# Kernel tuning notes

Measured on AMD Instinct MI355X. Metric: run time of the kernel, lower is better.

Reference implementation:

```python
import jax, jax.numpy as jnp
import numpy as np

BITS = 3
LEVELS = 2 ** BITS            # 8
HALF_RANGE = (LEVELS - 1) / 2  # 3.5
INCREMENT = 1.0 / (LEVELS // 2)  # 0.25


def setup_inputs() -> dict:
    key = jax.random.key(0)
    kq, kk, kv, kr = jax.random.split(key, 4)
    B, H, S, D = 2, 16, 2048, 128
    q = jax.random.normal(kq, (B, H, S, D), dtype=jnp.float32)
    k = jax.random.normal(kk, (B, H, S, D), dtype=jnp.float32)
    v = jax.random.normal(kv, (B, H, S, D), dtype=jnp.float32)
    # random orthogonal rotation (QR of a Gaussian), as in PolarQuant.__init__
    Hmat = jax.random.normal(kr, (D, D), dtype=jnp.float32)
    R, _ = jnp.linalg.qr(Hmat)
    qjl_scale = jnp.full((1,), 0.01, dtype=jnp.float32)
    return {"q": q, "k": k, "v": v, "R": R, "qjl_scale": qjl_scale}


def _compress_decompress(x, R, qjl_scale):
    """PolarQuant rotate -> QJL 3-bit quantize (+ sign correction) -> dequantize -> inverse rotate."""
    B, Hh, S, D = x.shape
    xr = jnp.einsum('bhsd,de->bhse', x, R)            # rotate: x @ R
    x_max = jnp.abs(xr).max() + 1e-8                   # global scale (as in quantize/compress)
    xs = xr / x_max * HALF_RANGE                       # scale to [-3.5, 3.5]
    xq = jnp.clip(jnp.round(xs / INCREMENT) * INCREMENT, -HALF_RANGE, HALF_RANGE)
    residual = xs - xq
    xc = xq + jnp.sign(residual) * qjl_scale[0] * x_max  # QJL 1-bit correction
    xd = xc / HALF_RANGE * x_max                       # dequantize
    xo = jnp.einsum('bhse,de->bhsd', xd, R)            # inverse rotate: y @ R.T
    return xo


def reference(q, k, v, R, qjl_scale):
    D = q.shape[-1]
    k_approx = _compress_decompress(k, R, qjl_scale)
    v_approx = _compress_decompress(v, R, qjl_scale)
    scores = jnp.einsum('bhqd,bhkd->bhqk', q, k_approx) / jnp.sqrt(jnp.float32(D))
    attn = jax.nn.softmax(scores, axis=-1)
    out = jnp.einsum('bhqk,bhkd->bhqd', attn, v_approx)
    return out
```

## Files before the change

### kernel.cpp

```cpp
#include <hip/hip_runtime.h>


typedef float    f32x4  __attribute__((ext_vector_type(4)));
typedef float    f32x16 __attribute__((ext_vector_type(16)));
typedef __bf16   bf16x8 __attribute__((ext_vector_type(8)));
typedef __bf16   bf16x4 __attribute__((ext_vector_type(4)));
typedef _Float16 f16x8  __attribute__((ext_vector_type(8)));
typedef unsigned long long u64;

#define SLEN 2048
#define DH   128

static __device__ __forceinline__ f32x16 zero16() {
  f32x16 z;
#pragma unroll
  for (int i = 0; i < 16; ++i) z[i] = 0.f;
  return z;
}

static __device__ __forceinline__ f32x16 mfma_bf16_32x32x16(bf16x8 a, bf16x8 b, f32x16 c) {
  return __builtin_amdgcn_mfma_f32_32x32x16_bf16(a, b, c, 0, 0, 0);
}
static __device__ __forceinline__ f32x16 mfma_f16_32x32x16(f16x8 a, f16x8 b, f32x16 c) {
  return __builtin_amdgcn_mfma_f32_32x32x16_f16(a, b, c, 0, 0, 0);
}

static __device__ __forceinline__ void lds_dma16(const void* g, void* l) {
  __builtin_amdgcn_global_load_lds(
      (const __attribute__((address_space(1))) void*)(unsigned long long)g,
      (__attribute__((address_space(3))) void*)(unsigned int)(unsigned long long)l,
      16, 0, 0);
}

static __device__ __forceinline__ float qdq(float xr, float xmax, float qs) {
  float xs = xr / xmax * 3.5f;
  float xq = rintf(xs * 4.0f) * 0.25f;
  xq = fminf(3.5f, fmaxf(-3.5f, xq));
  float res = xs - xq;
  float sg = (res > 0.0f) ? 1.0f : ((res < 0.0f) ? -1.0f : 0.0f);
  float xc = xq + sg * qs * xmax;
  return xc / 3.5f * xmax;
}

static __device__ __forceinline__ unsigned short bfbits(float f) {
  __bf16 b = (__bf16)f;
  return __builtin_bit_cast(unsigned short, b);
}

__global__ __launch_bounds__(256) void prep_R(
    const float* __restrict__ R, _Float16* __restrict__ Bhi,
    _Float16* __restrict__ Blo, _Float16* __restrict__ BhiT,
    _Float16* __restrict__ BloT)
{
  int i = blockIdx.x * 256 + threadIdx.x;
  int kk = i >> 7, n = i & 127;
  float r = R[i];
  _Float16 h = (_Float16)r;
  _Float16 l = (_Float16)(r - (float)h);
  Bhi[i] = h; Blo[i] = l;
  BhiT[n * 128 + kk] = h; BloT[n * 128 + kk] = l;
}

template<int NT, int MODE>
static __device__ __forceinline__ void rot_body(
    const float* __restrict__ X, const _Float16* __restrict__ Gh,
    const _Float16* __restrict__ Gl, void* __restrict__ OUTv,
    float* __restrict__ part, float* __restrict__ qn, int bid)
{
  __shared__ _Float16 BH[128 * 128];
  __shared__ _Float16 BL[(NT == 3) ? 128 * 128 : 8];

  const int tid = threadIdx.x, wave = tid >> 6, lane = tid & 63;
  const int r31 = lane & 31, hi = lane >> 5;
  const long r0 = (long)bid * 128;

#pragma unroll
  for (int u = 0; u < 8; ++u) {
    int c = (wave * 8 + u) * 64 + lane;
    int n = c >> 4, p = c & 15, ch = p ^ (n & 7);
    lds_dma16(Gh + n * 128 + ch * 8, BH + (wave * 8 + u) * 512);
    if constexpr (NT == 3)
      lds_dma16(Gl + n * 128 + ch * 8, BL + (wave * 8 + u) * 512);
  }

  const long rowg = r0 + wave * 32 + r31;
  f16x8 ah[8], al[8];
#pragma unroll
  for (int t = 0; t < 8; ++t) {
    f32x4 x0 = *(const f32x4*)&X[rowg * 128 + t * 16 + hi * 8];
    f32x4 x1 = *(const f32x4*)&X[rowg * 128 + t * 16 + hi * 8 + 4];
#pragma unroll
    for (int j = 0; j < 4; ++j) {
      _Float16 h0 = (_Float16)x0[j]; ah[t][j] = h0;
      _Float16 h1 = (_Float16)x1[j]; ah[t][4 + j] = h1;
      if constexpr (NT == 3) {
        al[t][j]     = (_Float16)(x0[j] - (float)h0);
        al[t][4 + j] = (_Float16)(x1[j] - (float)h1);
      }
    }
  }
  __syncthreads();

  f32x16 acc[4];
#pragma unroll
  for (int ct = 0; ct < 4; ++ct) acc[ct] = zero16();

#pragma unroll
  for (int ct = 0; ct < 4; ++ct) {
#pragma unroll
    for (int t = 0; t < 8; ++t) {
      int idx = (ct * 32 + r31) * 128 + (((2 * t + hi) ^ (r31 & 7)) * 8);
      f16x8 bh = *(const f16x8*)&BH[idx];
      acc[ct] = mfma_f16_32x32x16(ah[t], bh, acc[ct]);
      if constexpr (NT == 3) {
        f16x8 bl = *(const f16x8*)&BL[idx];
        acc[ct] = mfma_f16_32x32x16(ah[t], bl, acc[ct]);
        acc[ct] = mfma_f16_32x32x16(al[t], bh, acc[ct]);
      }
    }
  }

  if constexpr (MODE == 0) {
    float* OUT = (float*)OUTv;
    float am = 0.f;
#pragma unroll
    for (int ct = 0; ct < 4; ++ct)
#pragma unroll
      for (int r = 0; r < 16; ++r) {
        long grow = r0 + wave * 32 + (r & 3) + 8 * (r >> 2) + 4 * hi;
        float v = acc[ct][r];
        OUT[grow * 128 + ct * 32 + r31] = v;
        am = fmaxf(am, fabsf(v));
      }
#pragma unroll
    for (int m = 1; m <= 32; m <<= 1) am = fmaxf(am, __shfl_xor(am, m, 64));
    if (lane == 0) part[bid * 4 + wave] = am;
  } else if constexpr (MODE == 1) {
    __bf16* OUT = (__bf16*)OUTv;
    const float sc = 0.12751743342f;
    float rs[16];
#pragma unroll
    for (int r = 0; r < 16; ++r) rs[r] = 0.f;
#pragma unroll
    for (int ct = 0; ct < 4; ++ct)
#pragma unroll
      for (int r = 0; r < 16; ++r) {
        long grow = r0 + wave * 32 + (r & 3) + 8 * (r >> 2) + 4 * hi;
        __bf16 b = (__bf16)(acc[ct][r] * sc);
        OUT[grow * 128 + ct * 32 + r31] = b;
        float fb = (float)b;
        rs[r] += fb * fb;
      }
#pragma unroll
    for (int r = 0; r < 16; ++r) {
#pragma unroll
      for (int msk = 1; msk <= 16; msk <<= 1) rs[r] += __shfl_xor(rs[r], msk, 64);
      if (r31 == r)
        qn[r0 + wave * 32 + (r & 3) + 8 * (r >> 2) + 4 * hi] = sqrtf(rs[r]);
    }
  } else {
    float* OUT = (float*)OUTv;
#pragma unroll
    for (int ct = 0; ct < 4; ++ct)
#pragma unroll
      for (int r = 0; r < 16; ++r) {
        long grow = r0 + wave * 32 + (r & 3) + 8 * (r >> 2) + 4 * hi;
        OUT[grow * 128 + ct * 32 + r31] = acc[ct][r];
      }
  }
}

__global__ __launch_bounds__(256) void rot_kv_kernel(
    const float* __restrict__ K, const float* __restrict__ V,
    const _Float16* __restrict__ Gh, const _Float16* __restrict__ Gl,
    float* __restrict__ kr, float* __restrict__ vr,
    float* __restrict__ kpart, float* __restrict__ vpart)
{
  const bool isv = blockIdx.x >= 512;
  rot_body<3, 0>(isv ? V : K, Gh, Gl, isv ? (void*)vr : (void*)kr,
                 isv ? vpart : kpart, nullptr, blockIdx.x & 511);
}

__global__ __launch_bounds__(256) void rot_q_kernel(
    const float* __restrict__ X, const _Float16* __restrict__ Gh,
    const _Float16* __restrict__ Gl, __bf16* __restrict__ qb,
    float* __restrict__ qn)
{
  rot_body<1, 1>(X, Gh, Gl, (void*)qb, nullptr, qn, blockIdx.x);
}

__global__ __launch_bounds__(256) void rot_o_kernel(
    const float* __restrict__ X, const _Float16* __restrict__ Gh,
    const _Float16* __restrict__ Gl, float* __restrict__ out)
{
  rot_body<1, 2>(X, Gh, Gl, (void*)out, nullptr, nullptr, blockIdx.x);
}

__global__ __launch_bounds__(256) void quantize_vt_kernel(
    const float* __restrict__ vr, const float* __restrict__ vpart,
    const float* __restrict__ qjl, u64* __restrict__ vdt2)
{
  __shared__ unsigned int Ts32[128][18];
  __shared__ float sm[4];
  const int tid = threadIdx.x;

  float m = 0.f;
  for (int i = tid; i < 2048; i += 256) m = fmaxf(m, vpart[i]);
#pragma unroll
  for (int msk = 1; msk <= 32; msk <<= 1) m = fmaxf(m, __shfl_xor(m, msk, 64));
  if ((tid & 63) == 0) sm[tid >> 6] = m;
  __syncthreads();
  const float xmax = fmaxf(fmaxf(sm[0], sm[1]), fmaxf(sm[2], sm[3])) + 1e-8f;
  const float qs = qjl[0];

  const int bh = blockIdx.x >> 6, blk = blockIdx.x & 63;
  const int s0 = blk * 32;
  const int sp  = tid & 15;
  const int dch = tid >> 4;
  const long rb = (long)bh * SLEN + s0;
  const float* p0 = &vr[(rb + sp * 2    ) * 128 + dch * 8];
  const float* p1 = &vr[(rb + sp * 2 + 1) * 128 + dch * 8];
#pragma unroll
  for (int j = 0; j < 8; ++j) {
    unsigned a = bfbits(qdq(p0[j], xmax, qs));
    unsigned b = bfbits(qdq(p1[j], xmax, qs));
    Ts32[dch * 8 + j][sp] = a | (b << 16);
  }
  __syncthreads();
  const long obase = (long)(bh * 64 + blk) * 1024;
#pragma unroll
  for (int uu = 0; uu < 2; ++uu) {
    int u_ = uu * 256 + tid;
    int half = u_ >> 8, hi = (u_ >> 7) & 1, d = u_ & 127;
    u64 qlo = *(const u64*)&Ts32[d][2 * (half * 4 + hi)];
    u64 qhi = *(const u64*)&Ts32[d][2 * (half * 4 + hi + 2)];
    vdt2[obase + u_ * 2    ] = qlo;
    vdt2[obase + u_ * 2 + 1] = qhi;
  }
}

__global__ __launch_bounds__(256) void quantize_k_kernel(
    const float* __restrict__ kr, const float* __restrict__ kpart,
    const float* __restrict__ qjl, __bf16* __restrict__ out)
{
  __shared__ float sm[4];
  const int tid = threadIdx.x;
  float m = 0.f;
  for (int i = tid; i < 2048; i += 256) m = fmaxf(m, kpart[i]);
#pragma unroll
  for (int msk = 1; msk <= 32; msk <<= 1) m = fmaxf(m, __shfl_xor(m, msk, 64));
  if ((tid & 63) == 0) sm[tid >> 6] = m;
  __syncthreads();
  const float xmax = fmaxf(fmaxf(sm[0], sm[1]), fmaxf(sm[2], sm[3])) + 1e-8f;
  const float qs = qjl[0];

  long i = ((long)blockIdx.x * 256 + tid) * 4;
  f32x4 x = *(const f32x4*)&kr[i];
  bf16x4 ov;
#pragma unroll
  for (int j = 0; j < 4; ++j) ov[j] = (__bf16)qdq(x[j], xmax, qs);
  *(bf16x4*)&out[i] = ov;
}

__global__ __launch_bounds__(256, 2) void attn2(
    const __bf16* __restrict__ qb, const __bf16* __restrict__ kd,
    const u64* __restrict__ vdt2, const float* __restrict__ qn,
    const float* __restrict__ kpart, const float* __restrict__ qjl,
    float* __restrict__ orot)
{
  __shared__ __attribute__((aligned(16))) __bf16 Ks[2][2][32 * DH];
  __shared__ __attribute__((aligned(16))) u64   Vt[2][2][1024];
  __shared__ float Ls[4][32];
  __shared__ float sm[4];

  const int tid = threadIdx.x, wave = tid >> 6, lane = tid & 63;
  const int r31 = lane & 31, hi = lane >> 5;
  const int head = blockIdx.x & 31, qt = blockIdx.x >> 5;
  const long hrow = (long)head * SLEN;
  const int qrow0 = qt * 128 + wave * 32;

  float km = 0.f;
  for (int i = tid; i < 2048; i += 256) km = fmaxf(km, kpart[i]);
#pragma unroll
  for (int m = 1; m <= 32; m <<= 1) km = fmaxf(km, __shfl_xor(km, m, 64));
  if (lane == 0) sm[wave] = km;
  __syncthreads();
  const float xmax = fmaxf(fmaxf(sm[0], sm[1]), fmaxf(sm[2], sm[3])) + 1e-8f;
  const float Bk = 11.313708499f * ((3.5f + qjl[0] * xmax) * xmax / 3.5f) * 1.02f * 0.5f;

  bf16x8 qf[8];
#pragma unroll
  for (int t = 0; t < 8; ++t)
    qf[t] = *(const bf16x8*)&qb[(hrow + qrow0 + r31) * DH + t * 16 + hi * 8];
  const float mqneg = -(qn[hrow + qrow0 + r31] * Bk);

  int koff[8];
#pragma unroll
  for (int t = 0; t < 8; ++t)
    koff[t] = r31 * 256 + (((2 * t + hi) ^ (r31 & 7)) << 4);

  int vof0[4], vof1[4];
#pragma unroll
  for (int dt = 0; dt < 4; ++dt) {
    vof0[dt] = (((0 * 2 + hi) * 128) + dt * 32 + r31) * 16;
    vof1[dt] = (((1 * 2 + hi) * 128) + dt * 32 + r31) * 16;
  }

  const __bf16* ksrc[2]; int kds[2];
#pragma unroll
  for (int u = 0; u < 2; ++u) {
    int c = (wave * 2 + u) * 64 + lane;
    int row = c >> 4, ch = (c & 15) ^ (row & 7);
    ksrc[u] = kd + (hrow + row) * DH + ch * 8;
    kds[u] = (wave * 2 + u) * 512;
  }
  const char* vbase = (const char*)(vdt2 + (long)head * 64 * 1024);
  const char* vsrc[2];
#pragma unroll
  for (int u = 0; u < 2; ++u)
    vsrc[u] = vbase + (long)((wave * 2 + u) * 64 + lane) * 16;

  auto STAGE = [&](int B, int P) {
    const long k0 = (long)(2 * P) * 32 * DH, k1 = k0 + 32 * DH;
    const long v0 = (long)(2 * P) * 8192,    v1 = v0 + 8192;
    lds_dma16(ksrc[0] + k0, &Ks[B][0][kds[0]]);
    lds_dma16(ksrc[1] + k0, &Ks[B][0][kds[1]]);
    lds_dma16(ksrc[0] + k1, &Ks[B][1][kds[0]]);
    lds_dma16(ksrc[1] + k1, &Ks[B][1][kds[1]]);
    lds_dma16(vsrc[0] + v0, &Vt[B][0][(wave * 2 + 0) * 128]);
    lds_dma16(vsrc[1] + v0, &Vt[B][0][(wave * 2 + 1) * 128]);
    lds_dma16(vsrc[0] + v1, &Vt[B][1][(wave * 2 + 0) * 128]);
    lds_dma16(vsrc[1] + v1, &Vt[B][1][(wave * 2 + 1) * 128]);
  };

  STAGE(0, 0);
  STAGE(1, 1);
  asm volatile("s_waitcnt vmcnt(8)" ::: "memory");
  __builtin_amdgcn_s_barrier();
  asm volatile("" ::: "memory");

  f32x16 acc[4];
#pragma unroll
  for (int dt = 0; dt < 4; ++dt) acc[dt] = zero16();
  float ls0 = 0.f, ls1 = 0.f, ls2 = 0.f, ls3 = 0.f;

  auto TILE = [&](const f32x16& sa, const f32x16& sb, int B, int j) {
    float p[16];
#pragma unroll
    for (int r = 0; r < 16; ++r) p[r] = __builtin_amdgcn_exp2f(sa[r] + sb[r]);
#pragma unroll
    for (int r = 0; r < 16; r += 4) {
      ls0 += p[r]; ls1 += p[r + 1]; ls2 += p[r + 2]; ls3 += p[r + 3];
    }
    bf16x8 pa, pb;
#pragma unroll
    for (int jj = 0; jj < 8; ++jj) { pa[jj] = (__bf16)p[jj]; pb[jj] = (__bf16)p[8 + jj]; }
    const char* vb = (const char*)&Vt[B][j][0];
    __builtin_amdgcn_s_setprio(1);
#pragma unroll
    for (int dt = 0; dt < 4; ++dt) {
      bf16x8 v0 = *(const bf16x8*)(vb + vof0[dt]);
      acc[dt] = mfma_bf16_32x32x16(pa, v0, acc[dt]);
    }
#pragma unroll
    for (int dt = 0; dt < 4; ++dt) {
      bf16x8 v1 = *(const bf16x8*)(vb + vof1[dt]);
      acc[dt] = mfma_bf16_32x32x16(pb, v1, acc[dt]);
    }
    __builtin_amdgcn_s_setprio(0);
  };

#pragma unroll 1
  for (int i = 0; i < SLEN / 64; ++i) {
    const int B = i & 1;
    const char* k0 = (const char*)&Ks[B][0][0];
    const char* k1 = (const char*)&Ks[B][1][0];

    f32x16 sa0 = zero16(), sa1 = zero16(), sb0, sb1;
#pragma unroll
    for (int r = 0; r < 16; ++r) { sb0[r] = mqneg; sb1[r] = mqneg; }
    __builtin_amdgcn_s_setprio(1);
#pragma unroll
    for (int t = 0; t < 8; t += 2) {
      bf16x8 ka0 = *(const bf16x8*)(k0 + koff[t]);
      bf16x8 kb0 = *(const bf16x8*)(k1 + koff[t]);
      bf16x8 ka1 = *(const bf16x8*)(k0 + koff[t + 1]);
      bf16x8 kb1 = *(const bf16x8*)(k1 + koff[t + 1]);
      sa0 = mfma_bf16_32x32x16(ka0, qf[t], sa0);
      sa1 = mfma_bf16_32x32x16(kb0, qf[t], sa1);
      sb0 = mfma_bf16_32x32x16(ka1, qf[t + 1], sb0);
      sb1 = mfma_bf16_32x32x16(kb1, qf[t + 1], sb1);
    }
    __builtin_amdgcn_s_setprio(0);

    TILE(sa0, sb0, B, 0);
    TILE(sa1, sb1, B, 1);

    if (i < SLEN / 64 - 1) {
      asm volatile("s_waitcnt vmcnt(0)" ::: "memory");
      __builtin_amdgcn_s_barrier();
      asm volatile("" ::: "memory");
      if (i < SLEN / 64 - 2) STAGE(B, i + 2);
    }
  }

  float lsum = (ls0 + ls1) + (ls2 + ls3);
  lsum += __shfl_xor(lsum, 32, 64);
  if (hi == 0) Ls[wave][r31] = 1.0f / lsum;
  __syncthreads();

#pragma unroll
  for (int dt = 0; dt < 4; ++dt)
#pragma unroll
    for (int r = 0; r < 16; ++r) {
      int qr = (r & 3) + 8 * (r >> 2) + 4 * hi;
      orot[(hrow + qrow0 + qr) * DH + dt * 32 + r31] = acc[dt][r] * Ls[wave][qr];
    }
}

extern "C" void kernel_launch(void* const* d_in, const int* in_sizes, int n_in,
                              void* d_out, int out_size, void* d_ws, size_t ws_size,
                              hipStream_t stream)
{
  const float* q   = (const float*)d_in[0];
  const float* k   = (const float*)d_in[1];
  const float* v   = (const float*)d_in[2];
  const float* R   = (const float*)d_in[3];
  const float* qjl = (const float*)d_in[4];

  char* ws = (char*)d_ws;
  float* kpart = (float*)ws;
  float* vpart = (float*)(ws + 8192);
  _Float16* Bhi  = (_Float16*)(ws + 32768);
  _Float16* Blo  = (_Float16*)(ws + 65536);
  _Float16* BhiT = (_Float16*)(ws + 98304);
  _Float16* BloT = (_Float16*)(ws + 131072);
  float* qn = (float*)(ws + 163840);
  char* base = ws + 425984;
  __bf16* qb   = (__bf16*)base;
  float*  kr   = (float*)(base + (16u << 20));
  float*  vr   = (float*)(base + (48u << 20));
  u64*    vdt2 = (u64*)(base + (80u << 20));
  __bf16* kd   = (__bf16*)vr;
  float* orot  = kr;

  dim3 b256(256);
  prep_R<<<64, b256, 0, stream>>>(R, Bhi, Blo, BhiT, BloT);
  rot_kv_kernel<<<1024, b256, 0, stream>>>(k, v, BhiT, BloT, kr, vr, kpart, vpart);
  rot_q_kernel<<<512, b256, 0, stream>>>(q, BhiT, BloT, qb, qn);
  quantize_vt_kernel<<<2048, b256, 0, stream>>>(vr, vpart, qjl, vdt2);
  quantize_k_kernel<<<8192, b256, 0, stream>>>(kr, kpart, qjl, kd);
  attn2<<<512, b256, 0, stream>>>(qb, kd, vdt2, qn, kpart, qjl, orot);
  rot_o_kernel<<<512, b256, 0, stream>>>(orot, Bhi, Blo, (float*)d_out);
}
```

Baseline: 281.4 us.

## Fuse K/V/Q rotations into one kernel and store attention output as fp16

Merges the K/V and Q rotation kernels into a single launch. K/V blocks reuse one 32KB LDS buffer by loading the hi and lo halves of R in two phases, which lowers LDS per block and should allow more blocks per CU. The attention kernel now writes its rotated output as fp16 instead of fp32, and the output rotation reads it directly without converting from fp32. This halves that intermediate traffic at the cost of fp16 precision on the output before the final rotation.

```diff
diff --git a/kernel.cpp b/kernel.cpp
--- a/kernel.cpp
+++ b/kernel.cpp
@@ -61,67 +61,87 @@
   BhiT[n * 128 + kk] = h; BloT[n * 128 + kk] = l;
 }
 
-template<int NT, int MODE>
-static __device__ __forceinline__ void rot_body(
-    const float* __restrict__ X, const _Float16* __restrict__ Gh,
-    const _Float16* __restrict__ Gl, void* __restrict__ OUTv,
-    float* __restrict__ part, float* __restrict__ qn, int bid)
+__global__ __launch_bounds__(256) void rot_all_kernel(
+    const float* __restrict__ K, const float* __restrict__ V,
+    const float* __restrict__ Q, const _Float16* __restrict__ Gh,
+    const _Float16* __restrict__ Gl, float* __restrict__ kr,
+    float* __restrict__ vr, float* __restrict__ kpart,
+    float* __restrict__ vpart, __bf16* __restrict__ qb,
+    float* __restrict__ qn)
 {
   __shared__ _Float16 BH[128 * 128];
-  __shared__ _Float16 BL[(NT == 3) ? 128 * 128 : 8];
 
   const int tid = threadIdx.x, wave = tid >> 6, lane = tid & 63;
   const int r31 = lane & 31, hi = lane >> 5;
-  const long r0 = (long)bid * 128;
-
+  const int bid = blockIdx.x;
+
+  int stage_n[8], stage_ch[8], stage_dst[8];
 #pragma unroll
   for (int u = 0; u < 8; ++u) {
     int c = (wave * 8 + u) * 64 + lane;
-    int n = c >> 4, p = c & 15, ch = p ^ (n & 7);
-    lds_dma16(Gh + n * 128 + ch * 8, BH + (wave * 8 + u) * 512);
-    if constexpr (NT == 3)
-      lds_dma16(Gl + n * 128 + ch * 8, BL + (wave * 8 + u) * 512);
-  }
-
-  const long rowg = r0 + wave * 32 + r31;
-  f16x8 ah[8], al[8];
-#pragma unroll
-  for (int t = 0; t < 8; ++t) {
-    f32x4 x0 = *(const f32x4*)&X[rowg * 128 + t * 16 + hi * 8];
-    f32x4 x1 = *(const f32x4*)&X[rowg * 128 + t * 16 + hi * 8 + 4];
-#pragma unroll
-    for (int j = 0; j < 4; ++j) {
-      _Float16 h0 = (_Float16)x0[j]; ah[t][j] = h0;
-      _Float16 h1 = (_Float16)x1[j]; ah[t][4 + j] = h1;
-      if constexpr (NT == 3) {
+    stage_n[u] = c >> 4;
+    stage_ch[u] = (c & 15) ^ (stage_n[u] & 7);
+    stage_dst[u] = (wave * 8 + u) * 512;
+  }
+
+  if (bid < 1024) {
+    const bool isv = bid >= 512;
+    const int b = bid & 511;
+    const float* X = isv ? V : K;
+    float* OUT = isv ? vr : kr;
+    float* part = isv ? vpart : kpart;
+    const long r0 = (long)b * 128;
+
+#pragma unroll
+    for (int u = 0; u < 8; ++u)
+      lds_dma16(Gh + stage_n[u] * 128 + stage_ch[u] * 8, BH + stage_dst[u]);
+
+    const long rowg = r0 + wave * 32 + r31;
+    f16x8 ah[8], al[8];
+#pragma unroll
+    for (int t = 0; t < 8; ++t) {
+      f32x4 x0 = *(const f32x4*)&X[rowg * 128 + t * 16 + hi * 8];
+      f32x4 x1 = *(const f32x4*)&X[rowg * 128 + t * 16 + hi * 8 + 4];
+#pragma unroll
+      for (int j = 0; j < 4; ++j) {
+        _Float16 h0 = (_Float16)x0[j]; ah[t][j] = h0;
+        _Float16 h1 = (_Float16)x1[j]; ah[t][4 + j] = h1;
         al[t][j]     = (_Float16)(x0[j] - (float)h0);
         al[t][4 + j] = (_Float16)(x1[j] - (float)h1);
       }
     }
-  }
-  __syncthreads();
-
-  f32x16 acc[4];
-#pragma unroll
-  for (int ct = 0; ct < 4; ++ct) acc[ct] = zero16();
-
-#pragma unroll
-  for (int ct = 0; ct < 4; ++ct) {
-#pragma unroll
-    for (int t = 0; t < 8; ++t) {
-      int idx = (ct * 32 + r31) * 128 + (((2 * t + hi) ^ (r31 & 7)) * 8);
-      f16x8 bh = *(const f16x8*)&BH[idx];
-      acc[ct] = mfma_f16_32x32x16(ah[t], bh, acc[ct]);
-      if constexpr (NT == 3) {
-        f16x8 bl = *(const f16x8*)&BL[idx];
+    __syncthreads();
+
+    f32x16 acc[4];
+#pragma unroll
+    for (int ct = 0; ct < 4; ++ct) acc[ct] = zero16();
+#pragma unroll
+    for (int ct = 0; ct < 4; ++ct) {
+#pragma unroll
+      for (int t = 0; t < 8; ++t) {
+        int idx = (ct * 32 + r31) * 128 + (((2 * t + hi) ^ (r31 & 7)) * 8);
+        f16x8 bh = *(const f16x8*)&BH[idx];
+        acc[ct] = mfma_f16_32x32x16(ah[t], bh, acc[ct]);
+        acc[ct] = mfma_f16_32x32x16(al[t], bh, acc[ct]);
+      }
+    }
+
+    __syncthreads();
+#pragma unroll
+    for (int u = 0; u < 8; ++u)
+      lds_dma16(Gl + stage_n[u] * 128 + stage_ch[u] * 8, BH + stage_dst[u]);
+    __syncthreads();
+
+#pragma unroll
+    for (int ct = 0; ct < 4; ++ct) {
+#pragma unroll
+      for (int t = 0; t < 8; ++t) {
+        int idx = (ct * 32 + r31) * 128 + (((2 * t + hi) ^ (r31 & 7)) * 8);
+        f16x8 bl = *(const f16x8*)&BH[idx];
         acc[ct] = mfma_f16_32x32x16(ah[t], bl, acc[ct]);
-        acc[ct] = mfma_f16_32x32x16(al[t], bh, acc[ct]);
-      }
-    }
-  }
-
-  if constexpr (MODE == 0) {
-    float* OUT = (float*)OUTv;
+      }
+    }
+
     float am = 0.f;
 #pragma unroll
     for (int ct = 0; ct < 4; ++ct)
@@ -134,9 +154,43 @@
       }
 #pragma unroll
     for (int m = 1; m <= 32; m <<= 1) am = fmaxf(am, __shfl_xor(am, m, 64));
-    if (lane == 0) part[bid * 4 + wave] = am;
-  } else if constexpr (MODE == 1) {
-    __bf16* OUT = (__bf16*)OUTv;
+    if (lane == 0) part[b * 4 + wave] = am;
+
+  } else {
+    const int b = bid - 1024;
+    const long r0 = (long)b * 128;
+
+#pragma unroll
+    for (int u = 0; u < 8; ++u)
+      lds_dma16(Gh + stage_n[u] * 128 + stage_ch[u] * 8, BH + stage_dst[u]);
+
+    const long rowg = r0 + wave * 32 + r31;
+    f16x8 ah[8];
+#pragma unroll
+    for (int t = 0; t < 8; ++t) {
+      f32x4 x0 = *(const f32x4*)&Q[rowg * 128 + t * 16 + hi * 8];
+      f32x4 x1 = *(const f32x4*)&Q[rowg * 128 + t * 16 + hi * 8 + 4];
+#pragma unroll
+      for (int j = 0; j < 4; ++j) {
+        ah[t][j]     = (_Float16)x0[j];
+        ah[t][4 + j] = (_Float16)x1[j];
+      }
+    }
+    __syncthreads();
+
+    f32x16 acc[4];
+#pragma unroll
+    for (int ct = 0; ct < 4; ++ct) acc[ct] = zero16();
+#pragma unroll
+    for (int ct = 0; ct < 4; ++ct) {
+#pragma unroll
+      for (int t = 0; t < 8; ++t) {
+        int idx = (ct * 32 + r31) * 128 + (((2 * t + hi) ^ (r31 & 7)) * 8);
+        f16x8 bh = *(const f16x8*)&BH[idx];
+        acc[ct] = mfma_f16_32x32x16(ah[t], bh, acc[ct]);
+      }
+    }
+
     const float sc = 0.12751743342f;
     float rs[16];
 #pragma unroll
@@ -146,9 +200,9 @@
 #pragma unroll
       for (int r = 0; r < 16; ++r) {
         long grow = r0 + wave * 32 + (r & 3) + 8 * (r >> 2) + 4 * hi;
-        __bf16 b = (__bf16)(acc[ct][r] * sc);
-        OUT[grow * 128 + ct * 32 + r31] = b;
-        float fb = (float)b;
+        __bf16 bb = (__bf16)(acc[ct][r] * sc);
+        qb[grow * 128 + ct * 32 + r31] = bb;
+        float fb = (float)bb;
         rs[r] += fb * fb;
       }
 #pragma unroll
@@ -158,42 +212,52 @@
       if (r31 == r)
         qn[r0 + wave * 32 + (r & 3) + 8 * (r >> 2) + 4 * hi] = sqrtf(rs[r]);
     }
-  } else {
-    float* OUT = (float*)OUTv;
-#pragma unroll
-    for (int ct = 0; ct < 4; ++ct)
-#pragma unroll
-      for (int r = 0; r < 16; ++r) {
-        long grow = r0 + wave * 32 + (r & 3) + 8 * (r >> 2) + 4 * hi;
-        OUT[grow * 128 + ct * 32 + r31] = acc[ct][r];
-      }
-  }
-}
-
-__global__ __launch_bounds__(256) void rot_kv_kernel(
-    const float* __restrict__ K, const float* __restrict__ V,
-    const _Float16* __restrict__ Gh, const _Float16* __restrict__ Gl,
-    float* __restrict__ kr, float* __restrict__ vr,
-    float* __restrict__ kpart, float* __restrict__ vpart)
-{
-  const bool isv = blockIdx.x >= 512;
-  rot_body<3, 0>(isv ? V : K, Gh, Gl, isv ? (void*)vr : (void*)kr,
-                 isv ? vpart : kpart, nullptr, blockIdx.x & 511);
-}
-
-__global__ __launch_bounds__(256) void rot_q_kernel(
-    const float* __restrict__ X, const _Float16* __restrict__ Gh,
-    const _Float16* __restrict__ Gl, __bf16* __restrict__ qb,
-    float* __restrict__ qn)
-{
-  rot_body<1, 1>(X, Gh, Gl, (void*)qb, nullptr, qn, blockIdx.x);
+  }
 }
 
 __global__ __launch_bounds__(256) void rot_o_kernel(
-    const float* __restrict__ X, const _Float16* __restrict__ Gh,
-    const _Float16* __restrict__ Gl, float* __restrict__ out)
-{
-  rot_body<1, 2>(X, Gh, Gl, (void*)out, nullptr, nullptr, blockIdx.x);
+    const _Float16* __restrict__ X, const _Float16* __restrict__ Gh,
+    float* __restrict__ OUT)
+{
+  __shared__ _Float16 BH[128 * 128];
+
+  const int tid = threadIdx.x, wave = tid >> 6, lane = tid & 63;
+  const int r31 = lane & 31, hi = lane >> 5;
+  const long r0 = (long)blockIdx.x * 128;
+
+#pragma unroll
+  for (int u = 0; u < 8; ++u) {
+    int c = (wave * 8 + u) * 64 + lane;
+    int n = c >> 4, p = c & 15, ch = p ^ (n & 7);
+    lds_dma16(Gh + n * 128 + ch * 8, BH + (wave * 8 + u) * 512);
+  }
+
+  const long rowg = r0 + wave * 32 + r31;
+  f16x8 ah[8];
+#pragma unroll
+  for (int t = 0; t < 8; ++t)
+    ah[t] = *(const f16x8*)&X[rowg * 128 + t * 16 + hi * 8];
+  __syncthreads();
+
+  f32x16 acc[4];
+#pragma unroll
+  for (int ct = 0; ct < 4; ++ct) acc[ct] = zero16();
+#pragma unroll
+  for (int ct = 0; ct < 4; ++ct) {
+#pragma unroll
+    for (int t = 0; t < 8; ++t) {
+      int idx = (ct * 32 + r31) * 128 + (((2 * t + hi) ^ (r31 & 7)) * 8);
+      f16x8 bh = *(const f16x8*)&BH[idx];
+      acc[ct] = mfma_f16_32x32x16(ah[t], bh, acc[ct]);
+    }
+  }
+#pragma unroll
+  for (int ct = 0; ct < 4; ++ct)
+#pragma unroll
+    for (int r = 0; r < 16; ++r) {
+      long grow = r0 + wave * 32 + (r & 3) + 8 * (r >> 2) + 4 * hi;
+      OUT[grow * 128 + ct * 32 + r31] = acc[ct][r];
+    }
 }
 
 __global__ __launch_bounds__(256) void quantize_vt_kernel(
@@ -266,7 +330,7 @@
     const __bf16* __restrict__ qb, const __bf16* __restrict__ kd,
     const u64* __restrict__ vdt2, const float* __restrict__ qn,
     const float* __restrict__ kpart, const float* __restrict__ qjl,
-    float* __restrict__ orot)
+    _Float16* __restrict__ orot)
 {
   __shared__ __attribute__((aligned(16))) __bf16 Ks[2][2][32 * DH];
   __shared__ __attribute__((aligned(16))) u64   Vt[2][2][1024];
@@ -414,7 +478,8 @@
 #pragma unroll
     for (int r = 0; r < 16; ++r) {
       int qr = (r & 3) + 8 * (r >> 2) + 4 * hi;
-      orot[(hrow + qrow0 + qr) * DH + dt * 32 + r31] = acc[dt][r] * Ls[wave][qr];
+      orot[(hrow + qrow0 + qr) * DH + dt * 32 + r31] =
+          (_Float16)(acc[dt][r] * Ls[wave][qr]);
     }
 }
 
@@ -442,14 +507,14 @@
   float*  vr   = (float*)(base + (48u << 20));
   u64*    vdt2 = (u64*)(base + (80u << 20));
   __bf16* kd   = (__bf16*)vr;
-  float* orot  = kr;
+  _Float16* orot = (_Float16*)kr;
 
   dim3 b256(256);
   prep_R<<<64, b256, 0, stream>>>(R, Bhi, Blo, BhiT, BloT);
-  rot_kv_kernel<<<1024, b256, 0, stream>>>(k, v, BhiT, BloT, kr, vr, kpart, vpart);
-  rot_q_kernel<<<512, b256, 0, stream>>>(q, BhiT, BloT, qb, qn);
+  rot_all_kernel<<<1536, b256, 0, stream>>>(k, v, q, BhiT, BloT, kr, vr,
+                                            kpart, vpart, qb, qn);
   quantize_vt_kernel<<<2048, b256, 0, stream>>>(vr, vpart, qjl, vdt2);
   quantize_k_kernel<<<8192, b256, 0, stream>>>(kr, kpart, qjl, kd);
   attn2<<<512, b256, 0, stream>>>(qb, kd, vdt2, qn, kpart, qjl, orot);
-  rot_o_kernel<<<512, b256, 0, stream>>>(orot, Bhi, Blo, (float*)d_out);
-}
+  rot_o_kernel<<<512, b256, 0, stream>>>(orot, Bhi, (float*)d_out);
+}
```

New measurement: 274.4 us. 2.5% less time.
